# Optimization experiments

Hardware: AMD Instinct MI355X
Metric: run time of the kernel (lower is better)

Reference implementation:

```python
import jax, jax.numpy as jnp
import numpy as np

NUM_POSITIONS = 4096
EMBED_DIM = 512
BSZ, SEQ_LEN = 16, 4096


def setup_inputs() -> dict:
    key = jax.random.key(0)
    k1, k2 = jax.random.split(key)
    input_tensor = jax.random.normal(k1, (BSZ, SEQ_LEN, EMBED_DIM), dtype=jnp.float32)
    pv = jax.random.normal(k2, (NUM_POSITIONS, EMBED_DIM), dtype=jnp.float32)
    # L2-normalize each position vector (as in _init_position_vectors)
    pv = pv / jnp.linalg.norm(pv, axis=1, keepdims=True)
    return {"input_tensor": input_tensor, "position_vectors": pv}


def reference(input_tensor, position_vectors):
    # input_tensor: [B, S, D]; position_vectors: [P, D] with S <= P.
    seq_len, d = input_tensor.shape[1], input_tensor.shape[-1]
    pos = position_vectors[:seq_len]  # [S, D]
    # Batched circular convolution over the last axis via rFFT.
    x_fft = jnp.fft.rfft(input_tensor, axis=-1)          # [B, S, D//2+1] complex
    p_fft = jnp.fft.rfft(pos, axis=-1)[None, :, :]       # [1, S, D//2+1]
    out = jnp.fft.irfft(x_fft * p_fft, n=d, axis=-1)     # [B, S, D]
    return out.astype(input_tensor.dtype)
```

## Files before the change

kernel.cpp:

```cpp
#include <hip/hip_runtime.h>
#include <math.h>

#ifndef M_PI
#define M_PI 3.14159265358979323846
#endif

#define BSZ 16
#define SEQ 4096
#define DIM 512

__device__ __forceinline__ float2 cadd(float2 a, float2 b){ return make_float2(a.x+b.x, a.y+b.y); }
__device__ __forceinline__ float2 csub(float2 a, float2 b){ return make_float2(a.x-b.x, a.y-b.y); }
__device__ __forceinline__ float2 cmul(float2 a, float2 b){
  return make_float2(fmaf(a.x, b.x, -(a.y*b.y)), fmaf(a.x, b.y, a.y*b.x));
}
__device__ __forceinline__ float2 cmulc(float2 a, float2 b){
  return make_float2(fmaf(a.x, b.x, a.y*b.y), fmaf(a.y, b.x, -(a.x*b.y)));
}
__device__ __forceinline__ float2 mul_mi(float2 a){ return make_float2(a.y, -a.x); }

__device__ __forceinline__ void dft8(const float2* in, float2* out){
  float2 t0 = cadd(in[0], in[4]), t1 = csub(in[0], in[4]);
  float2 t2 = cadd(in[2], in[6]), t3 = csub(in[2], in[6]);
  float2 E0 = cadd(t0, t2), E2 = csub(t0, t2);
  float2 m3 = mul_mi(t3);
  float2 E1 = cadd(t1, m3), E3 = csub(t1, m3);
  float2 s0 = cadd(in[1], in[5]), s1 = csub(in[1], in[5]);
  float2 s2 = cadd(in[3], in[7]), s3 = csub(in[3], in[7]);
  float2 O0 = cadd(s0, s2), O2 = csub(s0, s2);
  float2 n3 = mul_mi(s3);
  float2 O1 = cadd(s1, n3), O3 = csub(s1, n3);
  const float C = 0.70710678118654752440f;
  float2 w1o = make_float2(C*(O1.x + O1.y), C*(O1.y - O1.x));
  float2 w2o = mul_mi(O2);
  float2 w3o = make_float2(C*(O3.y - O3.x), -(C*(O3.x + O3.y)));
  out[0] = cadd(E0, O0); out[4] = csub(E0, O0);
  out[1] = cadd(E1, w1o); out[5] = csub(E1, w1o);
  out[2] = cadd(E2, w2o); out[6] = csub(E2, w2o);
  out[3] = cadd(E3, w3o); out[7] = csub(E3, w3o);
}

__device__ __forceinline__ void idft8(const float2* in, float2* out){
  float2 t[8];
  dft8(in, t);
  out[0]=t[0]; out[1]=t[7]; out[2]=t[6]; out[3]=t[5];
  out[4]=t[4]; out[5]=t[3]; out[6]=t[2]; out[7]=t[1];
}

__device__ __forceinline__ void fft512_fwd(float2* v, float2* lds, int lane,
                                           const float2* wA, const float2* wB){
  const int r_hi = lane >> 3, r_lo = lane & 7;
  float2 t[8];
  dft8(v, t);
  #pragma unroll
  for (int r = 1; r < 8; ++r) t[r] = cmul(t[r], wA[r]);
  __syncthreads();
  #pragma unroll
  for (int r = 0; r < 8; ++r) lds[72*r + lane] = t[r];
  __syncthreads();
  #pragma unroll
  for (int j2 = 0; j2 < 8; ++j2) v[j2] = lds[72*r_hi + r_lo + 8*j2];
  dft8(v, t);
  #pragma unroll
  for (int r2 = 1; r2 < 8; ++r2) t[r2] = cmul(t[r2], wB[r2]);
  __syncthreads();
  #pragma unroll
  for (int r2 = 0; r2 < 8; ++r2) lds[r_hi + 72*r2 + 8*r_lo] = t[r2];
  __syncthreads();
  #pragma unroll
  for (int i2 = 0; i2 < 8; ++i2) v[i2] = lds[r_hi + 72*r_lo + 8*i2];
  dft8(v, t);
  #pragma unroll
  for (int m = 0; m < 8; ++m) v[m] = t[m];
}

__device__ __forceinline__ void fft512_inv(float2* v, float2* lds, int lane,
                                           const float2* wA, const float2* wB){
  const int r_hi = lane >> 3, r_lo = lane & 7;
  float2 t[8];
  idft8(v, t);
  __syncthreads();
  #pragma unroll
  for (int i2 = 0; i2 < 8; ++i2) lds[r_hi + 72*r_lo + 8*i2] = t[i2];
  __syncthreads();
  #pragma unroll
  for (int r2 = 0; r2 < 8; ++r2) v[r2] = lds[r_hi + 72*r2 + 8*r_lo];
  #pragma unroll
  for (int r2 = 1; r2 < 8; ++r2) v[r2] = cmulc(v[r2], wB[r2]);
  idft8(v, t);
  __syncthreads();
  #pragma unroll
  for (int j2 = 0; j2 < 8; ++j2) lds[72*r_hi + r_lo + 8*j2] = t[j2];
  __syncthreads();
  #pragma unroll
  for (int r = 0; r < 8; ++r) v[r] = lds[72*r + lane];
  #pragma unroll
  for (int r = 1; r < 8; ++r) v[r] = cmulc(v[r], wA[r]);
  idft8(v, t);
  #pragma unroll
  for (int j = 0; j < 8; ++j) v[j] = t[j];
}

__global__ void __launch_bounds__(64)
circconv_kernel(const float* __restrict__ x, const float* __restrict__ p,
                float* __restrict__ out){
  __shared__ float2 lds[576];
  const int lane = threadIdx.x;
  const int s = blockIdx.x;
  const int r_lo = lane & 7;

  float2 wA[8], wB[8];
  wA[0] = make_float2(1.f, 0.f); wB[0] = make_float2(1.f, 0.f);
  #pragma unroll
  for (int r = 1; r < 8; ++r){
    float sv, cv;
    sincosf(-2.0f*(float)M_PI*(float)(lane*r)*(1.0f/512.0f), &sv, &cv);
    wA[r] = make_float2(cv, sv);
    sincosf(-2.0f*(float)M_PI*(float)(r_lo*r)*(1.0f/64.0f), &sv, &cv);
    wB[r] = make_float2(cv, sv);
  }

  float2 pf[8];
  {
    const float* prow = p + (size_t)s * DIM;
    #pragma unroll
    for (int j = 0; j < 8; ++j) pf[j] = make_float2(prow[lane + 64*j], 0.f);
    fft512_fwd(pf, lds, lane, wA, wB);
    #pragma unroll
    for (int m = 0; m < 8; ++m){ pf[m].x *= (1.0f/512.0f); pf[m].y *= (1.0f/512.0f); }
  }

  for (int b = 0; b < BSZ; b += 2){
    const size_t base0 = ((size_t)b       * SEQ + s) * DIM;
    const size_t base1 = ((size_t)(b + 1) * SEQ + s) * DIM;
    float2 v[8];
    #pragma unroll
    for (int j = 0; j < 8; ++j)
      v[j] = make_float2(x[base0 + lane + 64*j], x[base1 + lane + 64*j]);
    fft512_fwd(v, lds, lane, wA, wB);
    #pragma unroll
    for (int m = 0; m < 8; ++m) v[m] = cmul(v[m], pf[m]);
    fft512_inv(v, lds, lane, wA, wB);
    #pragma unroll
    for (int j = 0; j < 8; ++j){
      out[base0 + lane + 64*j] = v[j].x;
      out[base1 + lane + 64*j] = v[j].y;
    }
  }
}

extern "C" void kernel_launch(void* const* d_in, const int* in_sizes, int n_in,
                              void* d_out, int out_size, void* d_ws, size_t ws_size,
                              hipStream_t stream) {
  (void)in_sizes; (void)n_in; (void)d_ws; (void)ws_size; (void)out_size;
  const float* x  = (const float*)d_in[0];
  const float* p  = (const float*)d_in[1];
  float* o        = (float*)d_out;
  circconv_kernel<<<SEQ, 64, 0, stream>>>(x, p, o);
}
```

Before: 243.9 us.

## Split batch across two waves per position, pack four waves per block, pad LDS

Each sequence position is now handled by two wavefronts, each covering half the batch, and four wavefronts share a 256-thread block with private LDS regions. The second-stage LDS transpose uses strides 82/10 instead of 72/8 to reduce bank conflicts. The aim is more parallelism and fewer small blocks, which should help latency hiding. The cost is that the position-vector FFT is computed twice per position, and each block uses more LDS.

```diff
diff --git a/kernel.cpp b/kernel.cpp
--- a/kernel.cpp
+++ b/kernel.cpp
@@ -8,6 +8,8 @@
 #define BSZ 16
 #define SEQ 4096
 #define DIM 512
+
+#define REG_SZ 656
 
 __device__ __forceinline__ float2 cadd(float2 a, float2 b){ return make_float2(a.x+b.x, a.y+b.y); }
 __device__ __forceinline__ float2 csub(float2 a, float2 b){ return make_float2(a.x-b.x, a.y-b.y); }
@@ -49,7 +51,7 @@
 
 __device__ __forceinline__ void fft512_fwd(float2* v, float2* lds, int lane,
                                            const float2* wA, const float2* wB){
-  const int r_hi = lane >> 3, r_lo = lane & 7;
+  const int a = lane >> 3, b = lane & 7;
   float2 t[8];
   dft8(v, t);
   #pragma unroll
@@ -59,16 +61,16 @@
   for (int r = 0; r < 8; ++r) lds[72*r + lane] = t[r];
   __syncthreads();
   #pragma unroll
-  for (int j2 = 0; j2 < 8; ++j2) v[j2] = lds[72*r_hi + r_lo + 8*j2];
+  for (int j2 = 0; j2 < 8; ++j2) v[j2] = lds[72*a + b + 8*j2];
   dft8(v, t);
   #pragma unroll
   for (int r2 = 1; r2 < 8; ++r2) t[r2] = cmul(t[r2], wB[r2]);
   __syncthreads();
   #pragma unroll
-  for (int r2 = 0; r2 < 8; ++r2) lds[r_hi + 72*r2 + 8*r_lo] = t[r2];
+  for (int r2 = 0; r2 < 8; ++r2) lds[a + 82*r2 + 10*b] = t[r2];
   __syncthreads();
   #pragma unroll
-  for (int i2 = 0; i2 < 8; ++i2) v[i2] = lds[r_hi + 72*r_lo + 8*i2];
+  for (int i2 = 0; i2 < 8; ++i2) v[i2] = lds[a + 82*b + 10*i2];
   dft8(v, t);
   #pragma unroll
   for (int m = 0; m < 8; ++m) v[m] = t[m];
@@ -76,21 +78,21 @@
 
 __device__ __forceinline__ void fft512_inv(float2* v, float2* lds, int lane,
                                            const float2* wA, const float2* wB){
-  const int r_hi = lane >> 3, r_lo = lane & 7;
+  const int a = lane >> 3, b = lane & 7;
   float2 t[8];
   idft8(v, t);
   __syncthreads();
   #pragma unroll
-  for (int i2 = 0; i2 < 8; ++i2) lds[r_hi + 72*r_lo + 8*i2] = t[i2];
+  for (int i2 = 0; i2 < 8; ++i2) lds[a + 82*b + 10*i2] = t[i2];
   __syncthreads();
   #pragma unroll
-  for (int r2 = 0; r2 < 8; ++r2) v[r2] = lds[r_hi + 72*r2 + 8*r_lo];
+  for (int r2 = 0; r2 < 8; ++r2) v[r2] = lds[a + 82*r2 + 10*b];
   #pragma unroll
   for (int r2 = 1; r2 < 8; ++r2) v[r2] = cmulc(v[r2], wB[r2]);
   idft8(v, t);
   __syncthreads();
   #pragma unroll
-  for (int j2 = 0; j2 < 8; ++j2) lds[72*r_hi + r_lo + 8*j2] = t[j2];
+  for (int j2 = 0; j2 < 8; ++j2) lds[72*a + b + 8*j2] = t[j2];
   __syncthreads();
   #pragma unroll
   for (int r = 0; r < 8; ++r) v[r] = lds[72*r + lane];
@@ -101,13 +103,18 @@
   for (int j = 0; j < 8; ++j) v[j] = t[j];
 }
 
-__global__ void __launch_bounds__(64)
+__global__ void __launch_bounds__(256)
 circconv_kernel(const float* __restrict__ x, const float* __restrict__ p,
                 float* __restrict__ out){
-  __shared__ float2 lds[576];
-  const int lane = threadIdx.x;
-  const int s = blockIdx.x;
-  const int r_lo = lane & 7;
+  __shared__ float2 lds_all[4 * REG_SZ];
+  const int lane = threadIdx.x & 63;
+  const int wid  = threadIdx.x >> 6;
+  float2* lds = lds_all + wid * REG_SZ;
+
+  const int g    = blockIdx.x * 4 + wid;
+  const int s    = g >> 1;
+  const int half = g & 1;
+  const int b    = lane & 7;
 
   float2 wA[8], wB[8];
   wA[0] = make_float2(1.f, 0.f); wB[0] = make_float2(1.f, 0.f);
@@ -116,7 +123,7 @@
     float sv, cv;
     sincosf(-2.0f*(float)M_PI*(float)(lane*r)*(1.0f/512.0f), &sv, &cv);
     wA[r] = make_float2(cv, sv);
-    sincosf(-2.0f*(float)M_PI*(float)(r_lo*r)*(1.0f/64.0f), &sv, &cv);
+    sincosf(-2.0f*(float)M_PI*(float)(b*r)*(1.0f/64.0f), &sv, &cv);
     wB[r] = make_float2(cv, sv);
   }
 
@@ -130,9 +137,10 @@
     for (int m = 0; m < 8; ++m){ pf[m].x *= (1.0f/512.0f); pf[m].y *= (1.0f/512.0f); }
   }
 
-  for (int b = 0; b < BSZ; b += 2){
-    const size_t base0 = ((size_t)b       * SEQ + s) * DIM;
-    const size_t base1 = ((size_t)(b + 1) * SEQ + s) * DIM;
+  const int b_lo = half * 8;
+  for (int bb = b_lo; bb < b_lo + 8; bb += 2){
+    const size_t base0 = ((size_t)bb       * SEQ + s) * DIM;
+    const size_t base1 = ((size_t)(bb + 1) * SEQ + s) * DIM;
     float2 v[8];
     #pragma unroll
     for (int j = 0; j < 8; ++j)
@@ -156,5 +164,5 @@
   const float* x  = (const float*)d_in[0];
   const float* p  = (const float*)d_in[1];
   float* o        = (float*)d_out;
-  circconv_kernel<<<SEQ, 64, 0, stream>>>(x, p, o);
+  circconv_kernel<<<SEQ*2/4, 256, 0, stream>>>(x, p, o);
 }
```

Result: no change. 243.0 us (-0.3%).
